# Optimization experiments

Measured on AMD Instinct MI355X. Metric: run time of the kernel, lower is better.

Reference implementation:

```python
import jax, jax.numpy as jnp
import numpy as np

N = 40000
IN_DIM = 2000
HID = 512
OUT_DIM = 30
E = 400000


def setup_inputs() -> dict:
    key = jax.random.key(0)
    k1, k2, k3, k4, k5, k6 = jax.random.split(key, 6)
    features = jax.random.normal(k1, (N, IN_DIM), dtype=jnp.float32)
    edge_index = jax.random.randint(k2, (2, E), 0, N, dtype=jnp.int64)
    # xavier_normal_(gain=1.414): std = gain * sqrt(2/(fan_in+fan_out))
    W1 = jax.random.normal(k3, (IN_DIM, HID), dtype=jnp.float32) * (1.414 * np.sqrt(2.0 / (IN_DIM + HID)))
    W2 = jax.random.normal(k4, (HID, OUT_DIM), dtype=jnp.float32) * (1.414 * np.sqrt(2.0 / (HID + OUT_DIM)))
    att_src = jax.random.normal(k5, (HID,), dtype=jnp.float32) * (1.414 * np.sqrt(2.0 / (1 + HID)))
    att_dst = jax.random.normal(k6, (HID,), dtype=jnp.float32) * (1.414 * np.sqrt(2.0 / (1 + HID)))
    return {"features": features, "W1": W1, "W2": W2,
            "att_src": att_src, "att_dst": att_dst, "edge_index": edge_index}


def _gat_propagate(x_proj, alpha_src, alpha_dst, src, dst, n_nodes):
    """GATConv message+aggregate (heads=1, aggr='add').
    x_proj: [N, C] projected features; alpha_src/alpha_dst: [N] per-node scores.
    """
    score = jax.nn.sigmoid(alpha_src[src] + alpha_dst[dst])          # [E]
    # segment softmax over destination neighborhoods (PyG softmax)
    seg_max = jax.ops.segment_max(score, dst, num_segments=n_nodes)  # [N]
    e = jnp.exp(score - seg_max[dst])                                # [E]
    seg_sum = jax.ops.segment_sum(e, dst, num_segments=n_nodes)     # [N]
    alpha = e / (seg_sum[dst] + 1e-16)                               # [E]
    msg = x_proj[src] * alpha[:, None]                               # [E, C] gather + scale
    return jax.ops.segment_sum(msg, dst, num_segments=n_nodes)      # [N, C] scatter-add


def _stagate_forward(features, W1, W2, att_src, att_dst, src, dst):
    n = features.shape[0]
    # conv1: attention=True (computes its own alpha)
    x1 = features @ W1                                # [N, HID]
    a_src = x1 @ att_src                              # [N]
    a_dst = x1 @ att_dst                              # [N]
    h1 = jax.nn.elu(_gat_propagate(x1, a_src, a_dst, src, dst, n))
    # conv2: attention=False -> just linear projection (heads=1 mean)
    h2 = h1 @ W2                                      # [N, OUT_DIM]
    # conv3: weights tied to W2^T, attention tied to conv1's alphas
    x3 = h2 @ W2.T                                    # [N, HID]
    h3 = jax.nn.elu(_gat_propagate(x3, a_src, a_dst, src, dst, n))
    # conv4: attention=False, weights tied to W1^T
    h4 = h3 @ W1.T                                    # [N, IN_DIM]
    return h2, h4


def reference(features, W1, W2, att_src, att_dst, edge_index):
    src = edge_index[0]
    dst = edge_index[1]
    return _stagate_forward(features, W1, W2, att_src, att_dst, src, dst)
```

## Files before the change

kernel.cpp:

```cpp
#include <hip/hip_runtime.h>
#include <cstdint>

#define NNODES 40000
#define INDIM 2000
#define HIDD 512
#define ODIM 30
#define NEDGES 400000
#define KPAD 2048

typedef short bf16x8 __attribute__((ext_vector_type(8)));
typedef float f32x4 __attribute__((ext_vector_type(4)));

__device__ __forceinline__ float bf2f(ushort u){ union{unsigned int i; float f;} x; x.i = ((unsigned int)u)<<16; return x.f; }
__device__ __forceinline__ ushort f2bf(float v){ union{float f; unsigned int u;} x; x.f=v; unsigned int r = x.u + 0x7fffu + ((x.u>>16)&1u); return (ushort)(r>>16); }

__global__ __launch_bounds__(256) void cast_feat_kernel(const float* __restrict__ src, ushort* __restrict__ dstb){
  int c = blockIdx.x*256 + threadIdx.x;
  int row = c >> 8, kc = c & 255;
  bf16x8 o;
  if (kc < INDIM/8) {
    const float* p = src + (size_t)row*INDIM + kc*8;
    #pragma unroll
    for (int j=0;j<8;++j) o[j] = (short)f2bf(p[j]);
  } else {
    #pragma unroll
    for (int j=0;j<8;++j) o[j] = 0;
  }
  *(bf16x8*)(dstb + (size_t)row*KPAD + kc*8) = o;
}

__global__ __launch_bounds__(256) void cast_w1_kernel(const float* __restrict__ W1, ushort* __restrict__ W1b, ushort* __restrict__ W1t){
  int idx = blockIdx.x*256 + threadIdx.x;
  if (idx >= INDIM*HIDD) return;
  int r = idx >> 9, c = idx & 511;
  ushort b = f2bf(W1[idx]);
  W1b[idx] = b;
  W1t[(size_t)c*KPAD + r] = b;
}

__global__ __launch_bounds__(256) void cast_w2_kernel(const float* __restrict__ W2, ushort* __restrict__ W2p, ushort* __restrict__ W2tc){
  int idx = blockIdx.x*256 + threadIdx.x;
  if (idx >= HIDD*32) return;
  int k = idx >> 5, c = idx & 31;
  float val = (c < ODIM) ? W2[k*ODIM + c] : 0.f;
  ushort b = f2bf(val);
  W2p[k*32 + c] = b;
  W2tc[c*HIDD + k] = b;
}

__global__ __launch_bounds__(256) void hist_kernel(const int* __restrict__ dst, int* __restrict__ deg){
  int e = blockIdx.x*256 + threadIdx.x;
  if (e < NEDGES) atomicAdd(&deg[dst[e]], 1);
}

__global__ __launch_bounds__(1024) void scan_kernel(const int* __restrict__ deg, int* __restrict__ row_ptr){
  __shared__ int part[1024];
  const int t = threadIdx.x;
  const int base = t * 40;
  int v[40];
  int s = 0;
  if (base < NNODES) {
    const int4* dp = (const int4*)(deg + base);
    #pragma unroll
    for (int j=0;j<10;++j){
      int4 d = dp[j];
      v[4*j+0] = s; s += d.x;
      v[4*j+1] = s; s += d.y;
      v[4*j+2] = s; s += d.z;
      v[4*j+3] = s; s += d.w;
    }
  } else {
    #pragma unroll
    for (int j=0;j<40;++j) v[j] = 0;
  }
  part[t] = s;
  __syncthreads();
  #pragma unroll
  for (int off=1; off<1024; off<<=1){
    int x = (t >= off) ? part[t-off] : 0;
    __syncthreads();
    part[t] += x;
    __syncthreads();
  }
  int offset = (t > 0) ? part[t-1] : 0;
  #pragma unroll
  for (int j=0;j<40;++j){
    int i = base + j;
    if (i <= NNODES) row_ptr[i] = offset + v[j];
  }
}

__global__ __launch_bounds__(256) void place_kernel(const int* __restrict__ src, const int* __restrict__ dst,
    const int* __restrict__ row_ptr, int* __restrict__ cursor, int* __restrict__ csr_src){
  int e = blockIdx.x*256 + threadIdx.x;
  if (e >= NEDGES) return;
  int d = dst[e];
  int pos = row_ptr[d] + atomicAdd(&cursor[d], 1);
  csr_src[pos] = src[e];
}

#define P_MID  asm volatile("" ::: "memory"); __builtin_amdgcn_s_barrier(); \
               asm volatile("s_waitcnt lgkmcnt(0)" ::: "memory"); \
               __builtin_amdgcn_sched_barrier(0); __builtin_amdgcn_s_setprio(1);
#define P_END  __builtin_amdgcn_s_setprio(0); asm volatile("" ::: "memory"); \
               __builtin_amdgcn_s_barrier(); __builtin_amdgcn_sched_barrier(0);
#define P_ENDW __builtin_amdgcn_s_setprio(0); \
               asm volatile("s_waitcnt vmcnt(4)" ::: "memory"); \
               asm volatile("" ::: "memory"); __builtin_amdgcn_s_barrier(); \
               __builtin_amdgcn_sched_barrier(0);

template<typename OutT>
__global__ __launch_bounds__(512, 2) void gemm8_kernel(
    const ushort* __restrict__ A, const ushort* __restrict__ Bt,
    OutT* __restrict__ C, int M, int N, int K, int ldc)
{
  __shared__ __align__(16) char smem[131072];
  ushort* Al = (ushort*)smem;
  ushort* Bl = (ushort*)(smem + 65536);
  const int tid = threadIdx.x;
  const int lane = tid & 63;
  const int w = tid >> 6;
  const int wm = w >> 2, wn = w & 3;
  const int row0 = blockIdx.y * 256;
  const int col0 = blockIdx.x * 256;
  const int NT = K >> 6;

  f32x4 acc[8][4] = {};
  bf16x8 a[4][2], b[4][2];

  auto stage = [&](bool isA, int kt, int h){
    const ushort* G = isA ? A : Bt;
    int base = isA ? row0 : col0;
    int lim  = isA ? M : N;
    ushort* L = (isA ? Al : Bl) + ((kt & 1) << 14);
    if (kt >= NT) kt -= NT;
    #pragma unroll
    for (int it = 0; it < 2; ++it){
      int ch = tid + (it << 9);
      int rl = (h << 7) + (ch >> 3);
      int cs = ch & 7;
      int gr = base + rl; gr = gr < lim ? gr : lim - 1;
      int gc = (kt << 6) + ((cs ^ (rl & 7)) << 3);
      __builtin_amdgcn_global_load_lds(
        (const __attribute__((address_space(1))) unsigned int*)(G + (size_t)gr*K + gc),
        (__attribute__((address_space(3))) unsigned int*)(L + rl*64 + cs*8), 16, 0, 0);
    }
  };
  auto lda = [&](int buf, int mf, int kk) -> bf16x8 {
    int rl = wm*128 + mf*16 + (lane & 15);
    int ko = kk*32 + ((lane >> 4) << 3);
    return *(const bf16x8*)&Al[(buf << 14) + rl*64 + (ko ^ ((rl & 7) << 3))];
  };
  auto ldb = [&](int buf, int nf, int kk) -> bf16x8 {
    int rl = wn*64 + nf*16 + (lane & 15);
    int ko = kk*32 + ((lane >> 4) << 3);
    return *(const bf16x8*)&Bl[(buf << 14) + rl*64 + (ko ^ ((rl & 7) << 3))];
  };
  auto mfma_q = [&](int mbase, int nbase){
    #pragma unroll
    for (int i=0;i<4;++i)
      #pragma unroll
      for (int j=0;j<2;++j)
        #pragma unroll
        for (int kk=0;kk<2;++kk)
          acc[mbase+i][nbase+j] = __builtin_amdgcn_mfma_f32_16x16x32_bf16(
              a[i][kk], b[nbase+j][kk], acc[mbase+i][nbase+j], 0, 0, 0);
  };

  stage(false, 0, 0); stage(false, 0, 1);
  stage(true , 0, 0); stage(true , 0, 1);
  stage(false, 1, 0); stage(false, 1, 1);
  asm volatile("s_waitcnt vmcnt(4)" ::: "memory");
  asm volatile("" ::: "memory");
  __builtin_amdgcn_s_barrier();
  __builtin_amdgcn_sched_barrier(0);

  const int NT2 = NT >> 1;
  for (int t = 0; t < NT2; ++t){
    const int kt0 = 2*t, kt1 = 2*t + 1;
    #pragma unroll
    for (int i=0;i<4;++i){ a[i][0]=lda(0,i,0); a[i][1]=lda(0,i,1); }
    #pragma unroll
    for (int j=0;j<2;++j){ b[j][0]=ldb(0,j,0); b[j][1]=ldb(0,j,1); }
    stage(true, kt1, 0);
    P_MID; mfma_q(0,0); P_END;
    #pragma unroll
    for (int j=2;j<4;++j){ b[j][0]=ldb(0,j,0); b[j][1]=ldb(0,j,1); }
    stage(true, kt1, 1);
    P_MID; mfma_q(0,2); P_END;
    #pragma unroll
    for (int i=0;i<4;++i){ a[i][0]=lda(0,4+i,0); a[i][1]=lda(0,4+i,1); }
    stage(false, kt0+2, 0);
    P_MID; mfma_q(4,0); P_END;
    stage(false, kt0+2, 1);
    P_MID; mfma_q(4,2); P_ENDW;
    #pragma unroll
    for (int i=0;i<4;++i){ a[i][0]=lda(1,i,0); a[i][1]=lda(1,i,1); }
    #pragma unroll
    for (int j=0;j<2;++j){ b[j][0]=ldb(1,j,0); b[j][1]=ldb(1,j,1); }
    stage(true, kt0+2, 0);
    P_MID; mfma_q(0,0); P_END;
    #pragma unroll
    for (int j=2;j<4;++j){ b[j][0]=ldb(1,j,0); b[j][1]=ldb(1,j,1); }
    stage(true, kt0+2, 1);
    P_MID; mfma_q(0,2); P_END;
    #pragma unroll
    for (int i=0;i<4;++i){ a[i][0]=lda(1,4+i,0); a[i][1]=lda(1,4+i,1); }
    stage(false, kt1+2, 0);
    P_MID; mfma_q(4,0); P_END;
    stage(false, kt1+2, 1);
    P_MID; mfma_q(4,2); P_ENDW;
  }

  asm volatile("s_waitcnt vmcnt(0)" ::: "memory");
  __syncthreads();

  if constexpr (sizeof(OutT)==2) {
    ushort* cs = (ushort*)smem;
    #pragma unroll
    for (int p=0;p<2;++p){
      if (wm == p){
        #pragma unroll
        for (int mf=0;mf<8;++mf)
          #pragma unroll
          for (int nf=0;nf<4;++nf)
            #pragma unroll
            for (int reg=0;reg<4;++reg)
              cs[(mf*16 + ((lane>>4)<<2) + reg)*264 + wn*64 + nf*16 + (lane&15)] = f2bf(acc[mf][nf][reg]);
      }
      __syncthreads();
      #pragma unroll
      for (int it=0; it<8; ++it){
        int ch = tid + it*512;
        int r = ch >> 5, c8 = (ch & 31) * 8;
        int gr = row0 + p*128 + r;
        if (gr < M && col0 + c8 + 8 <= N)
          *(bf16x8*)&((ushort*)C)[(size_t)gr*ldc + col0 + c8] = *(const bf16x8*)&cs[r*264 + c8];
      }
      __syncthreads();
    }
  } else {
    float* cf = (float*)smem;
    #pragma unroll
    for (int p=0;p<4;++p){
      if (wm == (p>>1)){
        int mh = (p & 1) * 4;
        #pragma unroll
        for (int i=0;i<4;++i)
          #pragma unroll
          for (int nf=0;nf<4;++nf)
            #pragma unroll
            for (int reg=0;reg<4;++reg)
              cf[(i*16 + ((lane>>4)<<2) + reg)*260 + wn*64 + nf*16 + (lane&15)] = acc[mh+i][nf][reg];
      }
      __syncthreads();
      #pragma unroll
      for (int it=0; it<8; ++it){
        int ch = tid + it*512;
        int r = ch >> 6, c4 = (ch & 63) * 4;
        int gr = row0 + p*64 + r, gc = col0 + c4;
        if (gr < M && gc + 4 <= N)
          *(f32x4*)&((float*)C)[(size_t)gr*ldc + gc] = *(const f32x4*)&cf[r*260 + c4];
      }
      __syncthreads();
    }
  }
}

__global__ __launch_bounds__(256) void a_kernel(const ushort* __restrict__ x1,
    const float* __restrict__ att_src, const float* __restrict__ att_dst,
    float* __restrict__ a_src, float* __restrict__ a_dst){
  int gid = blockIdx.x*256 + threadIdx.x;
  int row = gid >> 6, lane = gid & 63;
  if (row >= NNODES) return;
  bf16x8 v = *(const bf16x8*)(x1 + (size_t)row*HIDD + lane*8);
  float ps = 0.f, pd = 0.f;
  #pragma unroll
  for (int j=0;j<8;++j){
    float xv = bf2f((ushort)v[j]);
    ps += xv * att_src[lane*8+j];
    pd += xv * att_dst[lane*8+j];
  }
  #pragma unroll
  for (int off=32; off>0; off>>=1){ ps += __shfl_down(ps, off); pd += __shfl_down(pd, off); }
  if (lane == 0){ a_src[row] = ps; a_dst[row] = pd; }
}

__global__ __launch_bounds__(256) void alpha_kernel(const int* __restrict__ row_ptr,
    const int* __restrict__ csr_src, const float* __restrict__ a_src,
    const float* __restrict__ a_dst, float* __restrict__ csr_alpha){
  int gid = blockIdx.x*256 + threadIdx.x;
  int v = gid >> 4, lane = gid & 15;
  if (v >= NNODES) return;
  int p0 = row_ptr[v], p1 = row_ptr[v+1];
  if (p0 >= p1) return;
  float ad = a_dst[v];
  float m = -1e30f;
  for (int p = p0 + lane; p < p1; p += 16){
    float s = 1.f/(1.f + __expf(-(a_src[csr_src[p]] + ad)));
    m = fmaxf(m, s);
  }
  #pragma unroll
  for (int off=8; off>0; off>>=1) m = fmaxf(m, __shfl_xor(m, off));
  float sum = 0.f;
  for (int p = p0 + lane; p < p1; p += 16){
    float s = 1.f/(1.f + __expf(-(a_src[csr_src[p]] + ad)));
    float e = __expf(s - m);
    csr_alpha[p] = e;
    sum += e;
  }
  #pragma unroll
  for (int off=8; off>0; off>>=1) sum += __shfl_xor(sum, off);
  float inv = 1.f/(sum + 1e-16f);
  for (int p = p0 + lane; p < p1; p += 16) csr_alpha[p] *= inv;
}

__global__ __launch_bounds__(256) void agg_kernel(const ushort* __restrict__ X,
    const int* __restrict__ row_ptr, const int* __restrict__ csr_src,
    const float* __restrict__ csr_alpha, ushort* __restrict__ outb){
  __shared__ float red[3][64*8];
  int v = blockIdx.x;
  int lane = threadIdx.x & 63;
  int q = threadIdx.x >> 6;
  int p0 = row_ptr[v], p1 = row_ptr[v+1];
  float acc[8] = {0.f,0.f,0.f,0.f,0.f,0.f,0.f,0.f};
  for (int p = p0 + q; p < p1; p += 4){
    int s = csr_src[p];
    float al = csr_alpha[p];
    bf16x8 xv = *(const bf16x8*)(X + (size_t)s*HIDD + lane*8);
    #pragma unroll
    for (int j=0;j<8;++j) acc[j] += al * bf2f((ushort)xv[j]);
  }
  if (q > 0){
    #pragma unroll
    for (int j=0;j<8;++j) red[q-1][lane*8+j] = acc[j];
  }
  __syncthreads();
  if (q == 0){
    bf16x8 o;
    #pragma unroll
    for (int j=0;j<8;++j){
      float a = acc[j] + red[0][lane*8+j] + red[1][lane*8+j] + red[2][lane*8+j];
      a = a > 0.f ? a : __expf(a)-1.f;
      o[j] = (short)f2bf(a);
    }
    *(bf16x8*)(outb + (size_t)v*HIDD + lane*8) = o;
  }
}

__global__ __launch_bounds__(256) void mid_kernel(const ushort* __restrict__ h1,
    const ushort* __restrict__ W2tc, float* __restrict__ h2){
  __shared__ ushort h1s[32*512];
  __shared__ ushort w2s[32*512];
  const int t = threadIdx.x;
  const int row0 = blockIdx.x * 32;
  const ushort* g = h1 + (size_t)row0*HIDD;
  #pragma unroll
  for (int it=0; it<8; ++it){
    int ch = t + it*256;
    *(bf16x8*)&h1s[ch*8] = *(const bf16x8*)&g[ch*8];
    *(bf16x8*)&w2s[ch*8] = *(const bf16x8*)&W2tc[ch*8];
  }
  __syncthreads();
  int c = t & 31, rg = t >> 5;
  if (c < ODIM){
    float acc[4] = {0.f,0.f,0.f,0.f};
    for (int k0=0;k0<64;++k0){
      bf16x8 wv = *(const bf16x8*)&w2s[c*512 + k0*8];
      #pragma unroll
      for (int rr=0; rr<4; ++rr){
        bf16x8 hv = *(const bf16x8*)&h1s[(rg*4+rr)*HIDD + k0*8];
        #pragma unroll
        for (int j=0;j<8;++j) acc[rr] += bf2f((ushort)hv[j]) * bf2f((ushort)wv[j]);
      }
    }
    #pragma unroll
    for (int rr=0;rr<4;++rr) h2[(size_t)(row0 + rg*4 + rr)*ODIM + c] = acc[rr];
  }
}

__global__ __launch_bounds__(256) void agg30_kernel(const float* __restrict__ h2,
    const int* __restrict__ row_ptr, const int* __restrict__ csr_src,
    const float* __restrict__ csr_alpha, float* __restrict__ g){
  int gid = blockIdx.x*256 + threadIdx.x;
  int v = gid >> 5, lane = gid & 31;
  if (v >= NNODES) return;
  int p0 = row_ptr[v], p1 = row_ptr[v+1];
  float acc = 0.f;
  if (lane < ODIM){
    for (int p = p0; p < p1; ++p){
      acc += csr_alpha[p] * h2[(size_t)csr_src[p]*ODIM + lane];
    }
  }
  g[(size_t)v*32 + lane] = acc;
}

__global__ __launch_bounds__(256) void g2h3_kernel(const float* __restrict__ g,
    const ushort* __restrict__ W2p, ushort* __restrict__ h3){
  int gid = blockIdx.x*256 + threadIdx.x;
  int row = gid >> 6, lane = gid & 63;
  if (row >= NNODES) return;
  float h[ODIM];
  #pragma unroll
  for (int ci=0; ci<ODIM; ++ci) h[ci] = g[(size_t)row*32 + ci];
  #pragma unroll
  for (int it=0; it<8; ++it){
    int n = it*64 + lane;
    const ushort* wr = W2p + n*32;
    bf16x8 wvv[4];
    #pragma unroll
    for (int q=0;q<4;++q) wvv[q] = *(const bf16x8*)(wr + q*8);
    float acc = 0.f;
    #pragma unroll
    for (int ci=0; ci<ODIM; ++ci) acc += h[ci]*bf2f((ushort)wvv[ci>>3][ci&7]);
    acc = acc > 0.f ? acc : __expf(acc)-1.f;
    h3[(size_t)row*HIDD + n] = f2bf(acc);
  }
}

extern "C" void kernel_launch(void* const* d_in, const int* in_sizes, int n_in,
                              void* d_out, int out_size, void* d_ws, size_t ws_size,
                              hipStream_t stream){
  const float* features = (const float*)d_in[0];
  const float* W1 = (const float*)d_in[1];
  const float* W2 = (const float*)d_in[2];
  const float* att_src = (const float*)d_in[3];
  const float* att_dst = (const float*)d_in[4];
  const int* edge = (const int*)d_in[5];
  const int* esrc = edge;
  const int* edst = edge + NEDGES;

  float* h2 = (float*)d_out;
  float* h4 = h2 + (size_t)NNODES*ODIM;
  char* obase = (char*)h4;
  ushort* featb = (ushort*)obase;
  ushort* x1b   = (ushort*)(obase + 163840000);
  ushort* h1b   = (ushort*)(obase + 204800000);

  char* wbase = (char*)d_ws;
  size_t o = 0;
  auto walloc = [&](size_t bytes)->void*{ void* p = wbase + o; o += (bytes + 255) & ~(size_t)255; return p; };
  ushort* h3b      = (ushort*)walloc((size_t)NNODES*HIDD*2);
  ushort* W1b      = (ushort*)walloc((size_t)INDIM*HIDD*2);
  ushort* W1t      = (ushort*)walloc((size_t)HIDD*KPAD*2);
  ushort* W2p      = (ushort*)walloc(512*32*2);
  ushort* W2tc     = (ushort*)walloc(32*512*2);
  float*  a_src    = (float*)walloc(NNODES*4);
  float*  a_dst    = (float*)walloc(NNODES*4);
  int*    deg      = (int*)walloc(NNODES*4);
  int*    cursor   = (int*)walloc(NNODES*4);
  int*    row_ptr  = (int*)walloc((NNODES+1)*4);
  int*    csr_src  = (int*)walloc(NEDGES*4);
  float*  csr_alpha= (float*)walloc(NEDGES*4);
  float*  gbuf     = (float*)walloc((size_t)NNODES*32*4);

  hipMemsetAsync(deg, 0, NNODES*4, stream);
  hipMemsetAsync(cursor, 0, NNODES*4, stream);
  hipMemsetAsync(W1t, 0, (size_t)HIDD*KPAD*2, stream);

  cast_feat_kernel<<<40000, 256, 0, stream>>>(features, featb);
  cast_w1_kernel<<<(INDIM*HIDD+255)/256, 256, 0, stream>>>(W1, W1b, W1t);
  cast_w2_kernel<<<(HIDD*32+255)/256, 256, 0, stream>>>(W2, W2p, W2tc);
  hist_kernel<<<(NEDGES+255)/256, 256, 0, stream>>>(edst, deg);
  scan_kernel<<<1, 1024, 0, stream>>>(deg, row_ptr);
  place_kernel<<<(NEDGES+255)/256, 256, 0, stream>>>(esrc, edst, row_ptr, cursor, csr_src);

  gemm8_kernel<ushort><<<dim3(2, 157), 512, 0, stream>>>(featb, W1t, x1b, NNODES, HIDD, KPAD, HIDD);
  a_kernel<<<10000, 256, 0, stream>>>(x1b, att_src, att_dst, a_src, a_dst);
  alpha_kernel<<<2500, 256, 0, stream>>>(row_ptr, csr_src, a_src, a_dst, csr_alpha);
  agg_kernel<<<NNODES, 256, 0, stream>>>(x1b, row_ptr, csr_src, csr_alpha, h1b);
  mid_kernel<<<NNODES/32, 256, 0, stream>>>(h1b, W2tc, h2);
  agg30_kernel<<<NNODES*32/256, 256, 0, stream>>>(h2, row_ptr, csr_src, csr_alpha, gbuf);
  g2h3_kernel<<<10000, 256, 0, stream>>>(gbuf, W2p, h3b);
  gemm8_kernel<float><<<dim3(8, 157), 512, 0, stream>>>(h3b, W1b, h4, NNODES, INDIM, HIDD, INDIM);
}
```

Measured before the change: 679.3 us.

## Fuse attention softmax into aggregation and XCD-swizzle GEMM block order

Merges the per-destination softmax computation into the aggregation kernel. One wavefront computes the alphas into shared memory and still writes them to global memory for later reuse, which removes a separate launch and the re-read of alphas. Both GEMMs are also launched on a 1D grid with a swizzle that assigns neighbouring tiles to the same XCD, aiming at better L2 reuse. The cost is that the other three waves sit idle while the softmax runs, serialising that part of every block.

Result: no change. 682.6 us (+0.5%).

```diff
diff --git a/kernel.cpp b/kernel.cpp
--- a/kernel.cpp
+++ b/kernel.cpp
@@ -13,6 +13,13 @@
 
 __device__ __forceinline__ float bf2f(ushort u){ union{unsigned int i; float f;} x; x.i = ((unsigned int)u)<<16; return x.f; }
 __device__ __forceinline__ ushort f2bf(float v){ union{float f; unsigned int u;} x; x.f=v; unsigned int r = x.u + 0x7fffu + ((x.u>>16)&1u); return (ushort)(r>>16); }
+
+__device__ __forceinline__ int xcd_swz(int orig, int nwg){
+  int q = nwg >> 3, r = nwg & 7;
+  int xcd = orig & 7;
+  int idx = orig >> 3;
+  return (xcd < r ? xcd*(q+1) : r*(q+1) + (xcd-r)*q) + idx;
+}
 
 __global__ __launch_bounds__(256) void cast_feat_kernel(const float* __restrict__ src, ushort* __restrict__ dstb){
   int c = blockIdx.x*256 + threadIdx.x;
@@ -112,7 +119,7 @@
 template<typename OutT>
 __global__ __launch_bounds__(512, 2) void gemm8_kernel(
     const ushort* __restrict__ A, const ushort* __restrict__ Bt,
-    OutT* __restrict__ C, int M, int N, int K, int ldc)
+    OutT* __restrict__ C, int M, int N, int K, int ldc, int nwg, int cshift)
 {
   __shared__ __align__(16) char smem[131072];
   ushort* Al = (ushort*)smem;
@@ -121,8 +128,9 @@
   const int lane = tid & 63;
   const int w = tid >> 6;
   const int wm = w >> 2, wn = w & 3;
-  const int row0 = blockIdx.y * 256;
-  const int col0 = blockIdx.x * 256;
+  const int s = xcd_swz(blockIdx.x, nwg);
+  const int row0 = (s >> cshift) << 8;
+  const int col0 = (s & ((1 << cshift) - 1)) << 8;
   const int NT = K >> 6;
 
   f32x4 acc[8][4] = {};
@@ -286,48 +294,55 @@
   if (lane == 0){ a_src[row] = ps; a_dst[row] = pd; }
 }
 
-__global__ __launch_bounds__(256) void alpha_kernel(const int* __restrict__ row_ptr,
-    const int* __restrict__ csr_src, const float* __restrict__ a_src,
-    const float* __restrict__ a_dst, float* __restrict__ csr_alpha){
-  int gid = blockIdx.x*256 + threadIdx.x;
-  int v = gid >> 4, lane = gid & 15;
-  if (v >= NNODES) return;
-  int p0 = row_ptr[v], p1 = row_ptr[v+1];
-  if (p0 >= p1) return;
-  float ad = a_dst[v];
-  float m = -1e30f;
-  for (int p = p0 + lane; p < p1; p += 16){
-    float s = 1.f/(1.f + __expf(-(a_src[csr_src[p]] + ad)));
-    m = fmaxf(m, s);
-  }
-  #pragma unroll
-  for (int off=8; off>0; off>>=1) m = fmaxf(m, __shfl_xor(m, off));
-  float sum = 0.f;
-  for (int p = p0 + lane; p < p1; p += 16){
-    float s = 1.f/(1.f + __expf(-(a_src[csr_src[p]] + ad)));
-    float e = __expf(s - m);
-    csr_alpha[p] = e;
-    sum += e;
-  }
-  #pragma unroll
-  for (int off=8; off>0; off>>=1) sum += __shfl_xor(sum, off);
-  float inv = 1.f/(sum + 1e-16f);
-  for (int p = p0 + lane; p < p1; p += 16) csr_alpha[p] *= inv;
-}
-
-__global__ __launch_bounds__(256) void agg_kernel(const ushort* __restrict__ X,
+__global__ __launch_bounds__(256) void agg_fused_kernel(const ushort* __restrict__ X,
     const int* __restrict__ row_ptr, const int* __restrict__ csr_src,
-    const float* __restrict__ csr_alpha, ushort* __restrict__ outb){
+    const float* __restrict__ a_src, const float* __restrict__ a_dst,
+    float* __restrict__ csr_alpha, ushort* __restrict__ outb){
   __shared__ float red[3][64*8];
+  __shared__ float albuf[1024];
   int v = blockIdx.x;
   int lane = threadIdx.x & 63;
   int q = threadIdx.x >> 6;
   int p0 = row_ptr[v], p1 = row_ptr[v+1];
+  int deg = p1 - p0;
+
+  if (q == 0){
+    float ad = a_dst[v];
+    float m = -1e30f;
+    for (int i = lane; i < deg; i += 64){
+      float sc = 1.f/(1.f + __expf(-(a_src[csr_src[p0+i]] + ad)));
+      if (i < 1024) albuf[i] = sc;
+      m = fmaxf(m, sc);
+    }
+    #pragma unroll
+    for (int off=32; off>0; off>>=1) m = fmaxf(m, __shfl_xor(m, off));
+    float sum = 0.f;
+    for (int i = lane; i < deg; i += 64){
+      float sc = (i < 1024) ? albuf[i]
+               : 1.f/(1.f + __expf(-(a_src[csr_src[p0+i]] + ad)));
+      float e = __expf(sc - m);
+      if (i < 1024) albuf[i] = e;
+      sum += e;
+    }
+    #pragma unroll
+    for (int off=32; off>0; off>>=1) sum += __shfl_xor(sum, off);
+    float inv = 1.f/(sum + 1e-16f);
+    for (int i = lane; i < deg; i += 64){
+      float e = (i < 1024) ? albuf[i]
+              : __expf(1.f/(1.f + __expf(-(a_src[csr_src[p0+i]] + ad))) - m);
+      float al = e * inv;
+      if (i < 1024) albuf[i] = al;
+      csr_alpha[p0+i] = al;
+    }
+  }
+  __syncthreads();
+
   float acc[8] = {0.f,0.f,0.f,0.f,0.f,0.f,0.f,0.f};
   for (int p = p0 + q; p < p1; p += 4){
-    int s = csr_src[p];
-    float al = csr_alpha[p];
-    bf16x8 xv = *(const bf16x8*)(X + (size_t)s*HIDD + lane*8);
+    int i = p - p0;
+    int sidx = csr_src[p];
+    float al = (i < 1024) ? albuf[i] : csr_alpha[p];
+    bf16x8 xv = *(const bf16x8*)(X + (size_t)sidx*HIDD + lane*8);
     #pragma unroll
     for (int j=0;j<8;++j) acc[j] += al * bf2f((ushort)xv[j]);
   }
@@ -465,12 +480,11 @@
   scan_kernel<<<1, 1024, 0, stream>>>(deg, row_ptr);
   place_kernel<<<(NEDGES+255)/256, 256, 0, stream>>>(esrc, edst, row_ptr, cursor, csr_src);
 
-  gemm8_kernel<ushort><<<dim3(2, 157), 512, 0, stream>>>(featb, W1t, x1b, NNODES, HIDD, KPAD, HIDD);
+  gemm8_kernel<ushort><<<314, 512, 0, stream>>>(featb, W1t, x1b, NNODES, HIDD, KPAD, HIDD, 314, 1);
   a_kernel<<<10000, 256, 0, stream>>>(x1b, att_src, att_dst, a_src, a_dst);
-  alpha_kernel<<<2500, 256, 0, stream>>>(row_ptr, csr_src, a_src, a_dst, csr_alpha);
-  agg_kernel<<<NNODES, 256, 0, stream>>>(x1b, row_ptr, csr_src, csr_alpha, h1b);
+  agg_fused_kernel<<<NNODES, 256, 0, stream>>>(x1b, row_ptr, csr_src, a_src, a_dst, csr_alpha, h1b);
   mid_kernel<<<NNODES/32, 256, 0, stream>>>(h1b, W2tc, h2);
   agg30_kernel<<<NNODES*32/256, 256, 0, stream>>>(h2, row_ptr, csr_src, csr_alpha, gbuf);
   g2h3_kernel<<<10000, 256, 0, stream>>>(gbuf, W2p, h3b);
-  gemm8_kernel<float><<<dim3(8, 157), 512, 0, stream>>>(h3b, W1b, h4, NNODES, INDIM, HIDD, INDIM);
-}
+  gemm8_kernel<float><<<1256, 512, 0, stream>>>(h3b, W1b, h4, NNODES, INDIM, HIDD, INDIM, 1256, 3);
+}
```
